# Performance work log

Hardware: AMD Instinct MI355X
Metric: run time of the kernel (lower is better)

Reference implementation:

```python
import jax, jax.numpy as jnp
import numpy as np

B, C, H, W = 16, 256, 96, 96
CQ = C // 8      # 32, query/key channels in CrossAttention
CM = C // 2      # 128, inter_planes


def conv1x1(x, w, b=None):
    # x: [B,Cin,H,W], w: [Cout,Cin]
    y = jnp.einsum('bchw,oc->bohw', x, w)
    if b is not None:
        y = y + b[None, :, None, None]
    return y


def cross_attention(x, wq, bq, wk, bk, wv, bv, gamma):
    # criss-cross (axial H and W) attention with -inf diagonal on the H branch
    b_, c_, h_, w_ = x.shape
    q = conv1x1(x, wq, bq)  # [B,CQ,H,W]
    k = conv1x1(x, wk, bk)
    v = conv1x1(x, wv, bv)  # [B,C,H,W]
    # energy over column (H axis): [B,H,W,H], masked diag h==h'
    e_h = jnp.einsum('bchw,bckw->bhwk', q, k)
    diag = jnp.eye(h_, dtype=bool)[None, :, None, :]  # [1,H,1,H]
    e_h = jnp.where(diag, -jnp.inf, e_h)
    # energy over row (W axis): [B,H,W,W]
    e_w = jnp.einsum('bchw,bchv->bhwv', q, k)
    att = jax.nn.softmax(jnp.concatenate([e_h, e_w], axis=3), axis=3)
    a_h, a_w = att[..., :h_], att[..., h_:]
    out_h = jnp.einsum('bckw,bhwk->bchw', v, a_h)
    out_w = jnp.einsum('bchv,bhwv->bchw', v, a_w)
    return gamma * (out_h + out_w) + x


def spatial_weighted(x, w_q_right, w_v_right, w_up, b_up):
    b_, _, h_, w_ = x.shape
    inp = conv1x1(x, w_v_right).reshape(b_, CM, h_ * w_)        # [B,CM,HW]
    mask = conv1x1(x, w_q_right).reshape(b_, 1, h_ * w_)        # [B,1,HW]
    mask = jax.nn.softmax(mask, axis=2)
    ctx = jnp.einsum('bcn,bon->bco', inp, mask)                 # [B,CM,1]
    ctx = jnp.einsum('bci,oc->boi', ctx, w_up) + b_up[None, :, None]  # [B,C,1]
    mask_ch = jax.nn.sigmoid(ctx)[..., None]                    # [B,C,1,1]
    return x * mask_ch


def channel_weighted(x, w_q_left, w_v_left):
    b_, _, h_, w_ = x.shape
    g = conv1x1(x, w_q_left)                                    # [B,CM,H,W]
    avg = jnp.mean(g, axis=(2, 3))                              # [B,CM]
    theta = conv1x1(x, w_v_left).reshape(b_, CM, h_ * w_)       # [B,CM,HW]
    ctx = jnp.einsum('bc,bcn->bn', avg, theta)                  # [B,HW]
    ctx = jax.nn.softmax(ctx, axis=1).reshape(b_, 1, h_, w_)
    return x * jax.nn.sigmoid(ctx)


def setup_inputs() -> dict:
    key = jax.random.key(0)
    ks = jax.random.split(key, 16)
    s = lambda fan_in: (2.0 / fan_in) ** 0.5
    inp = {
        'x': jax.random.normal(ks[0], (B, C, H, W), jnp.float32),
        'w_q_right': jax.random.normal(ks[1], (1, C), jnp.float32) * s(C),
        'w_v_right': jax.random.normal(ks[2], (CM, C), jnp.float32) * s(C),
        'w_up': jax.random.normal(ks[3], (C, CM), jnp.float32) * s(CM),
        'b_up': jnp.zeros((C,), jnp.float32),
        'w_q_left': jax.random.normal(ks[4], (CM, C), jnp.float32) * s(C),
        'w_v_left': jax.random.normal(ks[5], (CM, C), jnp.float32) * s(C),
        'cr_wq': jax.random.normal(ks[6], (CQ, C), jnp.float32) * s(C),
        'cr_bq': jnp.zeros((CQ,), jnp.float32),
        'cr_wk': jax.random.normal(ks[7], (CQ, C), jnp.float32) * s(C),
        'cr_bk': jnp.zeros((CQ,), jnp.float32),
        'cr_wv': jax.random.normal(ks[8], (C, C), jnp.float32) * s(C),
        'cr_bv': jnp.zeros((C,), jnp.float32),
        'gamma': jax.random.normal(ks[9], (1,), jnp.float32) * 0.1,
    }
    return inp


def reference(x, w_q_right, w_v_right, w_up, b_up, w_q_left, w_v_left,
              cr_wq, cr_bq, cr_wk, cr_bk, cr_wv, cr_bv, gamma):
    cross = lambda t: cross_attention(t, cr_wq, cr_bq, cr_wk, cr_bk, cr_wv, cr_bv, gamma)
    ctx_channel = cross(spatial_weighted(x, w_q_right, w_v_right, w_up, b_up))
    ctx_spatial = cross(channel_weighted(x, w_q_left, w_v_left))
    return cross(ctx_spatial + ctx_channel)
```

## Files before the change

kernel.cpp:

```cpp
#include <hip/hip_runtime.h>
#include <math.h>

#define Bn 16
#define Cn 256
#define Hn 96
#define Wn 96
#define Nn 9216
#define PIXn 147456
#define XSZk ((size_t)Bn*Cn*Nn)
#define YSZk ((size_t)Bn*64*Nn)
#define ATTSZ ((size_t)PIXn*96)

typedef short bf8 __attribute__((ext_vector_type(8)));
typedef float f32x4 __attribute__((ext_vector_type(4)));
#define MFMA(a,b,c) __builtin_amdgcn_mfma_f32_16x16x32_bf16(a,b,c,0,0,0)

typedef unsigned short ushort_t;
typedef _Float16 h16;

__device__ inline ushort_t f2bf(float f){
  union{float f; unsigned int u;} v; v.f=f;
  unsigned int r = v.u + 0x7fffu + ((v.u>>16)&1u);
  return (ushort_t)(r>>16);
}
__device__ inline float bf2f(ushort_t s){
  union{unsigned int u; float f;} v; v.u = ((unsigned int)s)<<16;
  return v.f;
}
__device__ inline ushort_t f2h(float f){
  union{h16 h; ushort_t u;} v; v.h=(h16)f; return v.u;
}
__device__ inline float h2f(ushort_t u){
  union{ushort_t u; h16 h;} v; v.u=u; return (float)v.h;
}

__device__ inline float waveSum(float v){
#pragma unroll
  for(int o=32;o;o>>=1) v += __shfl_down(v,o,64);
  return v;
}
__device__ inline float waveMax(float v){
#pragma unroll
  for(int o=32;o;o>>=1) v = fmaxf(v,__shfl_down(v,o,64));
  return v;
}


template<int XBW>
__global__ __launch_bounds__(1024) void k_pass1(const float* __restrict__ x,
    const float* __restrict__ wqr, float* __restrict__ xmean,
    float* __restrict__ partp, ushort_t* __restrict__ XB){
  int cg = blockIdx.x, b = blockIdx.y, tid = threadIdx.x;
  __shared__ float r16[16];
  float mp[2][8];
#pragma unroll
  for(int u=0;u<2;u++)
#pragma unroll
    for(int e=0;e<8;e++) mp[u][e]=0.f;
  for(int cc=0;cc<16;cc++){
    int c = cg*16+cc;
    const float* row = x + ((size_t)b*Cn + c)*Nn;
    float w = wqr[c];
    float s = 0.f;
#pragma unroll
    for(int u=0;u<2;u++){
      int ch = tid + u*1024;
      if(ch < 1152){
        float4 a = *(const float4*)&row[ch*8];
        float4 d = *(const float4*)&row[ch*8+4];
        float v0=a.x,v1=a.y,v2=a.z,v3=a.w,v4=d.x,v5=d.y,v6=d.z,v7=d.w;
        s += ((v0+v1)+(v2+v3))+((v4+v5)+(v6+v7));
        mp[u][0]+=w*v0; mp[u][1]+=w*v1; mp[u][2]+=w*v2; mp[u][3]+=w*v3;
        mp[u][4]+=w*v4; mp[u][5]+=w*v5; mp[u][6]+=w*v6; mp[u][7]+=w*v7;
        if(XBW){
          uint4 pk;
          pk.x=(unsigned)f2bf(v0)|((unsigned)f2bf(v1)<<16);
          pk.y=(unsigned)f2bf(v2)|((unsigned)f2bf(v3)<<16);
          pk.z=(unsigned)f2bf(v4)|((unsigned)f2bf(v5)<<16);
          pk.w=(unsigned)f2bf(v6)|((unsigned)f2bf(v7)<<16);
          *(uint4*)&XB[((size_t)b*Cn + c)*Nn + ch*8] = pk;
        }
      }
    }
    s = waveSum(s);
    if((tid&63)==0) r16[tid>>6]=s;
    __syncthreads();
    if(tid==0){
      float t=0.f;
      for(int i=0;i<16;i++) t+=r16[i];
      xmean[(size_t)b*Cn + c] = t*(1.f/Nn);
    }
    __syncthreads();
  }
  float* dst = partp + ((size_t)cg*Bn + b)*Nn;
#pragma unroll
  for(int u=0;u<2;u++){
    int ch = tid + u*1024;
    if(ch < 1152){
      float4 o1, o2;
      o1.x=mp[u][0]; o1.y=mp[u][1]; o1.z=mp[u][2]; o1.w=mp[u][3];
      o2.x=mp[u][4]; o2.y=mp[u][5]; o2.z=mp[u][6]; o2.w=mp[u][7];
      *(float4*)&dst[ch*8]   = o1;
      *(float4*)&dst[ch*8+4] = o2;
    }
  }
}

template<int XBR>
__global__ __launch_bounds__(1024) void k_pass2(const float* __restrict__ x,
    const ushort_t* __restrict__ XB, const float* __restrict__ wvec,
    const float* __restrict__ maskb, float* __restrict__ xw,
    float* __restrict__ partp){
  int cg = blockIdx.x, b = blockIdx.y, tid = threadIdx.x;
  __shared__ float r16[16];
  float cp[2][8], mk[2][8];
#pragma unroll
  for(int u=0;u<2;u++){
    int ch = tid + u*1024;
    if(ch < 1152){
      float4 a = *(const float4*)&maskb[(size_t)b*Nn + ch*8];
      float4 d = *(const float4*)&maskb[(size_t)b*Nn + ch*8 + 4];
      mk[u][0]=a.x; mk[u][1]=a.y; mk[u][2]=a.z; mk[u][3]=a.w;
      mk[u][4]=d.x; mk[u][5]=d.y; mk[u][6]=d.z; mk[u][7]=d.w;
    }
#pragma unroll
    for(int e=0;e<8;e++) cp[u][e]=0.f;
  }
  for(int cc=0;cc<16;cc++){
    int c = cg*16+cc;
    float w = wvec[(size_t)b*Cn + c];
    float s = 0.f;
#pragma unroll
    for(int u=0;u<2;u++){
      int ch = tid + u*1024;
      if(ch < 1152){
        float v[8];
        if(XBR){
          uint4 q = *(const uint4*)&XB[((size_t)b*Cn + c)*Nn + ch*8];
          unsigned* qp=(unsigned*)&q;
#pragma unroll
          for(int k=0;k<4;k++){
            v[2*k]   = bf2f((ushort_t)(qp[k]&0xffff));
            v[2*k+1] = bf2f((ushort_t)(qp[k]>>16));
          }
        } else {
          const float* row = x + ((size_t)b*Cn + c)*Nn;
          float4 a = *(const float4*)&row[ch*8];
          float4 d = *(const float4*)&row[ch*8+4];
          v[0]=a.x; v[1]=a.y; v[2]=a.z; v[3]=a.w;
          v[4]=d.x; v[5]=d.y; v[6]=d.z; v[7]=d.w;
        }
#pragma unroll
        for(int e=0;e<8;e++){
          s += mk[u][e]*v[e];
          cp[u][e] += w*v[e];
        }
      }
    }
    s = waveSum(s);
    if((tid&63)==0) r16[tid>>6]=s;
    __syncthreads();
    if(tid==0){
      float t=0.f;
      for(int i=0;i<16;i++) t+=r16[i];
      xw[(size_t)b*Cn + c] = t;
    }
    __syncthreads();
  }
  float* dst = partp + ((size_t)cg*Bn + b)*Nn;
#pragma unroll
  for(int u=0;u<2;u++){
    int ch = tid + u*1024;
    if(ch < 1152){
      float4 o1, o2;
      o1.x=cp[u][0]; o1.y=cp[u][1]; o1.z=cp[u][2]; o1.w=cp[u][3];
      o2.x=cp[u][4]; o2.y=cp[u][5]; o2.z=cp[u][6]; o2.w=cp[u][7];
      *(float4*)&dst[ch*8]   = o1;
      *(float4*)&dst[ch*8+4] = o2;
    }
  }
}

__global__ void k_red16(const float* __restrict__ part, float* __restrict__ out){
  size_t p = (size_t)blockIdx.x*256 + threadIdx.x;
  float s=0.f;
#pragma unroll
  for(int cg=0;cg<16;cg++) s += part[(size_t)cg*Bn*Nn + p];
  out[p]=s;
}

__device__ inline void softmax_n_body(const float* __restrict__ in,
    float* __restrict__ out, int b, int mode){
  int tid=threadIdx.x, lane=tid&63, wid=tid>>6;
  const float* p = in + (size_t)b*Nn;
  __shared__ float red[16];
  __shared__ float bc2[2];
  float mx=-3e38f;
  for(int i=tid;i<Nn;i+=1024) mx=fmaxf(mx,p[i]);
  mx = waveMax(mx);
  if(lane==0) red[wid]=mx;
  __syncthreads();
  if(tid==0){ float m=red[0]; for(int i=1;i<16;i++) m=fmaxf(m,red[i]); bc2[0]=m; }
  __syncthreads();
  mx=bc2[0];
  float s=0.f;
  for(int i=tid;i<Nn;i+=1024) s+=expf(p[i]-mx);
  s = waveSum(s);
  __syncthreads();
  if(lane==0) red[wid]=s;
  __syncthreads();
  if(tid==0){ float t=0.f; for(int i=0;i<16;i++) t+=red[i]; bc2[1]=t; }
  __syncthreads();
  float inv=1.f/bc2[1];
  for(int i=tid;i<Nn;i+=1024){
    float e=expf(p[i]-mx)*inv;
    out[(size_t)b*Nn+i] = mode ? 1.f/(1.f+expf(-e)) : e;
  }
}

__global__ __launch_bounds__(1024) void k_sn1(const float* __restrict__ mraw,
    float* __restrict__ maskb, const float* __restrict__ xmean,
    const float* __restrict__ wql, const float* __restrict__ wvl,
    float* __restrict__ wvec){
  if(blockIdx.x < 16){
    softmax_n_body(mraw, maskb, blockIdx.x, 0);
  } else {
    int b = blockIdx.x - 16, t = threadIdx.x;
    __shared__ float xm[Cn];
    __shared__ float av[128];
    if(t<Cn) xm[t] = xmean[b*Cn+t];
    __syncthreads();
    if(t<128){
      float s=0.f;
      for(int c=0;c<Cn;c++) s += wql[t*Cn+c]*xm[c];
      av[t]=s;
    }
    __syncthreads();
    if(t<Cn){
      float s=0.f;
      for(int m=0;m<128;m++) s += av[m]*wvl[m*Cn+t];
      wvec[b*Cn+t]=s;
    }
  }
}

__global__ __launch_bounds__(1024) void k_sn2(const float* __restrict__ craw,
    float* __restrict__ m2, const float* __restrict__ xw,
    const float* __restrict__ wvr, const float* __restrict__ wup,
    const float* __restrict__ bup, float* __restrict__ g1){
  if(blockIdx.x < 16){
    softmax_n_body(craw, m2, blockIdx.x, 1);
  } else {
    int b = blockIdx.x - 16, t = threadIdx.x;
    __shared__ float xs[Cn];
    __shared__ float cx[128];
    if(t<Cn) xs[t]=xw[b*Cn+t];
    __syncthreads();
    if(t<128){
      float s=0.f;
      for(int c=0;c<Cn;c++) s += wvr[t*Cn+c]*xs[c];
      cx[t]=s;
    }
    __syncthreads();
    if(t<Cn){
      float s=bup[t];
      for(int m=0;m<128;m++) s += wup[t*128+m]*cx[m];
      g1[b*Cn+t]=1.f/(1.f+expf(-s));
    }
  }
}


__global__ void k_packb(const float* __restrict__ wq, const float* __restrict__ bq,
                        const float* __restrict__ wk, const float* __restrict__ bk,
                        const float* __restrict__ wv, const float* __restrict__ bv,
                        ushort_t* __restrict__ Wp, float* __restrict__ bp){
  int o = blockIdx.x, t = threadIdx.x;
  const float* src; float bs;
  if(o<32){ src = wq + o*Cn; bs = bq[o]; }
  else if(o<64){ src = wk + (o-32)*Cn; bs = bk[o-32]; }
  else { src = wv + (o-64)*Cn; bs = bv[o-64]; }
  Wp[o*Cn+t] = f2bf(src[t]);
  if(t==0) bp[o] = bs;
}

#define AP 40
#define BP 264
#define GP 68

template<int GATED, int XBR>
__global__ __launch_bounds__(256) void k_gemm_qkv(
    const ushort_t* __restrict__ tb, const float* __restrict__ x,
    const ushort_t* __restrict__ XBp,
    const float* __restrict__ g1, const float* __restrict__ m2,
    const ushort_t* __restrict__ Wp, const float* __restrict__ bp,
    ushort_t* __restrict__ Yqk, ushort_t* __restrict__ Vb, int sel){
  __shared__ ushort_t SM[320*AP + 64*BP];
  __shared__ float gsh[256];
  ushort_t* Ws = SM;
  ushort_t* Bt = SM + 320*AP;
  int b = blockIdx.y;
  int n0 = blockIdx.x*64;
  int tid = threadIdx.x, lane = tid&63, wid = tid>>6;

  if(GATED){
    gsh[tid] = g1[b*Cn + tid];
    __syncthreads();
    float scl_n = (sel==1) ? m2[(size_t)b*Nn + n0 + (tid&63)] : 0.f;
    int cg = (tid>>6)*8;
#pragma unroll
    for(int p=0;p<8;p++){
      int c8 = p*32 + cg;
      float fv[8];
      if(XBR){
        const ushort_t* xb = XBp + (size_t)b*Cn*Nn + n0 + (tid&63);
#pragma unroll
        for(int k2=0;k2<8;k2++){
          float xf = bf2f(xb[(size_t)(c8+k2)*Nn]);
          fv[k2] = xf * (sel==0 ? gsh[c8+k2] : scl_n);
        }
      } else {
        const float* xb = x + (size_t)b*Cn*Nn + n0 + (tid&63);
#pragma unroll
        for(int k2=0;k2<8;k2++){
          float xf = xb[(size_t)(c8+k2)*Nn];
          fv[k2] = xf * (sel==0 ? gsh[c8+k2] : scl_n);
        }
      }
      uint4 pk;
      pk.x = (unsigned)f2bf(fv[0]) | ((unsigned)f2bf(fv[1])<<16);
      pk.y = (unsigned)f2bf(fv[2]) | ((unsigned)f2bf(fv[3])<<16);
      pk.z = (unsigned)f2bf(fv[4]) | ((unsigned)f2bf(fv[5])<<16);
      pk.w = (unsigned)f2bf(fv[6]) | ((unsigned)f2bf(fv[7])<<16);
      *(uint4*)&Bt[(tid&63)*BP + c8] = pk;
    }
  } else {
    const ushort_t* xb = tb + (size_t)b*Cn*Nn + n0 + (tid&63);
    int cg = (tid>>6)*8;
#pragma unroll
    for(int p=0;p<8;p++){
      int c8 = p*32 + cg;
      unsigned e0=xb[(size_t)(c8+0)*Nn], e1=xb[(size_t)(c8+1)*Nn];
      unsigned e2=xb[(size_t)(c8+2)*Nn], e3=xb[(size_t)(c8+3)*Nn];
      unsigned e4=xb[(size_t)(c8+4)*Nn], e5=xb[(size_t)(c8+5)*Nn];
      unsigned e6=xb[(size_t)(c8+6)*Nn], e7=xb[(size_t)(c8+7)*Nn];
      uint4 pk;
      pk.x = e0 | (e1<<16); pk.y = e2 | (e3<<16);
      pk.z = e4 | (e5<<16); pk.w = e6 | (e7<<16);
      *(uint4*)&Bt[(tid&63)*BP + c8] = pk;
    }
  }

  f32x4 acc[5][4];
#pragma unroll
  for(int f=0;f<5;f++)
#pragma unroll
    for(int g=0;g<4;g++) acc[f][g] = (f32x4){0.f,0.f,0.f,0.f};

  for(int ki=0;ki<8;ki++){
    __syncthreads();
#pragma unroll
    for(int q=0;q<5;q++){
      int fidx = q*256 + tid;
      int o = fidx>>2, kk = (fidx&3)*8;
      uint4 wv = *(const uint4*)&Wp[o*Cn + ki*32 + kk];
      *(uint4*)&Ws[o*AP + kk] = wv;
    }
    __syncthreads();
    bf8 bfr[4];
#pragma unroll
    for(int g=0;g<4;g++)
      bfr[g] = *(const bf8*)&Bt[(g*16 + (lane&15))*BP + ki*32 + (lane>>4)*8];
#pragma unroll
    for(int f=0;f<5;f++){
      bf8 a = *(const bf8*)&Ws[(wid*80 + f*16 + (lane&15))*AP + (lane>>4)*8];
#pragma unroll
      for(int g=0;g<4;g++) acc[f][g] = MFMA(a, bfr[g], acc[f][g]);
    }
  }

  __syncthreads();
#pragma unroll
  for(int f=0;f<5;f++){
    int o = wid*80 + f*16 + (lane>>4)*4;
#pragma unroll
    for(int i=0;i<4;i++){
      float bias = bp[o+i];
#pragma unroll
      for(int g=0;g<4;g++)
        SM[(o+i)*GP + g*16 + (lane&15)] = f2bf(acc[f][g][i] + bias);
    }
  }
  __syncthreads();
  for(int u=tid; u<320*8; u+=256){
    int lo_ = u>>3, c8 = (u&7)*8;
    ushort_t* dst = (lo_<64) ? (Yqk + ((size_t)b*64 + lo_)*Nn)
                             : (Vb + ((size_t)b*Cn + (lo_-64))*Nn);
    *(uint4*)&dst[n0 + c8] = *(uint4*)&SM[lo_*GP + c8];
  }
}

__global__ __launch_bounds__(256) void k_transpose_b(const ushort_t* __restrict__ src,
                                                     ushort_t* __restrict__ dst){
  __shared__ ushort_t Ls[96*98];
  size_t base = (size_t)blockIdx.x * Nn;
  int tid = threadIdx.x;
  for(int e=tid*2; e<Nn; e+=512){
    unsigned int u = *(const unsigned int*)&src[base+e];
    int r=e/96, c=e%96;
    *(unsigned int*)&Ls[r*98+c] = u;
  }
  __syncthreads();
  for(int e=tid*2; e<Nn; e+=512){
    int r=e/96, c=e%96;
    unsigned int u = (unsigned int)Ls[c*98+r] | (((unsigned int)Ls[(c+1)*98+r])<<16);
    *(unsigned int*)&dst[base+e] = u;
  }
}

__global__ __launch_bounds__(256) void k_e2(const ushort_t* __restrict__ Yqk,
    const ushort_t* __restrict__ Yqkt, ushort_t* __restrict__ attl,
    ushort_t* __restrict__ attr){
  __shared__ ushort_t Qt[96*AP];
  __shared__ ushort_t Kt[96*AP];
  int r = blockIdx.x, mode = blockIdx.y, b = blockIdx.z;
  const ushort_t* Y = mode ? Yqk : Yqkt;
  int pm   = mode ? 1  : 96;
  int pr   = mode ? 96 : 1;
  ushort_t* attx = mode ? attr : attl;
  int tid = threadIdx.x, lane = tid&63, wid = tid>>6;
  {
    int half = tid>>7;
    int cg   = (tid>>5)&3;
    int l32  = tid&31;
    ushort_t* T = half ? Kt : Qt;
    const ushort_t* S = Y + ((size_t)b*64 + half*32 + cg*8)*Nn + (size_t)r*96;
#pragma unroll
    for(int p=0;p<3;p++){
      int sp = p*32 + l32;
      unsigned e0=S[(size_t)0*Nn+sp], e1=S[(size_t)1*Nn+sp];
      unsigned e2=S[(size_t)2*Nn+sp], e3=S[(size_t)3*Nn+sp];
      unsigned e4=S[(size_t)4*Nn+sp], e5=S[(size_t)5*Nn+sp];
      unsigned e6=S[(size_t)6*Nn+sp], e7=S[(size_t)7*Nn+sp];
      uint4 pk;
      pk.x = e0 | (e1<<16); pk.y = e2 | (e3<<16);
      pk.z = e4 | (e5<<16); pk.w = e6 | (e7<<16);
      *(uint4*)&T[sp*AP + cg*8] = pk;
    }
  }
  __syncthreads();
  int mb = (wid>>1)*48, nb = (wid&1)*48;
  const f32x4 z4 = {0.f,0.f,0.f,0.f};
  f32x4 acc[3][3];
  bf8 a[3], bb[3];
#pragma unroll
  for(int f=0;f<3;f++) a[f] = *(const bf8*)&Qt[(mb+f*16+(lane&15))*AP + (lane>>4)*8];
#pragma unroll
  for(int g=0;g<3;g++) bb[g] = *(const bf8*)&Kt[(nb+g*16+(lane&15))*AP + (lane>>4)*8];
#pragma unroll
  for(int f=0;f<3;f++)
#pragma unroll
    for(int g=0;g<3;g++) acc[f][g] = MFMA(a[f], bb[g], z4);
#pragma unroll
  for(int f=0;f<3;f++)
#pragma unroll
    for(int i=0;i<4;i++){
      int m = mb + f*16 + (lane>>4)*4 + i;
      ushort_t* arow = attx + ((size_t)b*Nn + (size_t)m*pm + (size_t)r*pr)*96;
#pragma unroll
      for(int g=0;g<3;g++){
        int n = nb + g*16 + (lane&15);
        arow[n] = f2h(acc[f][g][i]);
      }
    }
}

__global__ __launch_bounds__(256) void k_smvt(ushort_t* attl, ushort_t* attr,
    const ushort_t* __restrict__ Vsrc, ushort_t* __restrict__ Vdst){
  __shared__ ushort_t Ls[96*98];
  int b = blockIdx.z;
  if(blockIdx.x < 1164){
    int wave = threadIdx.x>>6, l = threadIdx.x&63;
    int t = blockIdx.x*4 + wave;
    int i=0, base=0;
    while(base + (96-i) <= t){ base += 96-i; i++; }
    int j = i + (t-base);
    int hf = l>>5, l32 = l&31;
    int h = hf ? j : i, w = hf ? i : j;
    size_t p = (size_t)b*Nn + (size_t)h*96 + w;
    const ushort_t* al = attl + p*96;
    const ushort_t* ar = attr + p*96;
    float v[6];
#pragma unroll
    for(int k=0;k<3;k++){
      int el = l32 + 32*k;
      float vv = h2f(al[el]);
      v[k] = (el==h) ? -1e30f : vv;
    }
#pragma unroll
    for(int k=0;k<3;k++) v[3+k] = h2f(ar[l32 + 32*k]);
    float mx = v[0];
#pragma unroll
    for(int k=1;k<6;k++) mx = fmaxf(mx, v[k]);
#pragma unroll
    for(int o=16;o;o>>=1) mx = fmaxf(mx, __shfl_xor(mx, o, 64));
    float e[6], s=0.f;
#pragma unroll
    for(int k=0;k<6;k++){ e[k]=expf(v[k]-mx); s+=e[k]; }
#pragma unroll
    for(int o=16;o;o>>=1) s += __shfl_xor(s, o, 64);
    float inv = 1.f/s;
    size_t q = (size_t)b*Nn + (size_t)w*96 + h;
    ushort_t* oh = attl + q*96;
    ushort_t* ow = attr + p*96;
#pragma unroll
    for(int k=0;k<3;k++) oh[l32+32*k] = f2bf(e[k]*inv);
#pragma unroll
    for(int k=0;k<3;k++) ow[l32+32*k] = f2bf(e[3+k]*inv);
  } else {
    int c = blockIdx.x - 1164;
    size_t base = ((size_t)b*Cn + c) * Nn;
    int tid = threadIdx.x;
    for(int e=tid*2; e<Nn; e+=512){
      unsigned int u = *(const unsigned int*)&Vsrc[base+e];
      int r=e/96, cc=e%96;
      *(unsigned int*)&Ls[r*98+cc] = u;
    }
    __syncthreads();
    for(int e=tid*2; e<Nn; e+=512){
      int r=e/96, cc=e%96;
      unsigned int u = (unsigned int)Ls[cc*98+r] | (((unsigned int)Ls[(cc+1)*98+r])<<16);
      *(unsigned int*)&Vdst[base+e] = u;
    }
  }
}

#define SP 104
#define RP 100

template<int RES, int XBR>
__global__ __launch_bounds__(256) void k_pv2(const ushort_t* __restrict__ VB,
    const ushort_t* __restrict__ VTb, const ushort_t* __restrict__ attw,
    const ushort_t* __restrict__ atth, const float* __restrict__ x,
    const ushort_t* __restrict__ XBp,
    const float* __restrict__ g1, const float* __restrict__ m2,
    const ushort_t* __restrict__ residb, ushort_t* __restrict__ Tob,
    ushort_t* __restrict__ OTb, const float* __restrict__ gp, int sel){
  __shared__ ushort_t SMEM[96*SP];
  int r = blockIdx.x, mode = blockIdx.y>>2, q4 = blockIdx.y&3, b = blockIdx.z;
  float gm = gp[0];
  int tid = threadIdx.x, lane = tid&63, wid = tid>>6;
  const ushort_t* V = mode ? VTb : VB;
  size_t vbase = (size_t)b*Cn*Nn + (size_t)r*96;
  int cb = q4*64 + wid*16;
  const ushort_t* ab = (mode ? atth : attw) + ((size_t)b*Nn + (size_t)r*96)*96;
  for(int u=tid; u<96*12; u+=256){
    int n=u/12, j8=(u%12)*8;
    uint4 qv = *(const uint4*)&ab[n*96 + j8];
    *(uint4*)&SMEM[n*SP + j8] = qv;
  }
  __syncthreads();
  f32x4 acc[6];
#pragma unroll
  for(int g=0;g<6;g++) acc[g] = (f32x4){0.f,0.f,0.f,0.f};
#pragma unroll
  for(int j0=0;j0<3;j0++){
    bf8 vf = *(const bf8*)&V[vbase
        + (size_t)(cb + (lane&15))*Nn + j0*32 + (lane>>4)*8];
    bf8 bfr[6];
#pragma unroll
    for(int g=0;g<6;g++)
      bfr[g] = *(const bf8*)&SMEM[(g*16+(lane&15))*SP + j0*32 + (lane>>4)*8];
#pragma unroll
    for(int g=0;g<6;g++) acc[g] = MFMA(vf, bfr[g], acc[g]);
  }
  __syncthreads();
  {
    int rl = wid*16 + (lane>>4)*4;
#pragma unroll
    for(int i=0;i<4;i++)
#pragma unroll
      for(int g=0;g<6;g++)
        SMEM[(rl+i)*RP + g*16 + (lane&15)] = f2bf(gm*acc[g][i]);
  }
  __syncthreads();
  for(int u=tid; u<64*12; u+=256){
    int rl = u/12, q8 = (u%12)*8;
    int c = q4*64 + rl;
    size_t row = vbase + (size_t)c*Nn;
    uint4 v = *(uint4*)&SMEM[rl*RP + q8];
    if(mode){
      *(uint4*)&OTb[row + q8] = v;
    } else {
      unsigned* vp=(unsigned*)&v;
      float rs[8];
      if(RES==1){
        uint4 rv = *(const uint4*)&residb[row + q8];
        unsigned* rp=(unsigned*)&rv;
#pragma unroll
        for(int k=0;k<4;k++){
          rs[2*k]   = bf2f((ushort_t)(rp[k]&0xffff));
          rs[2*k+1] = bf2f((ushort_t)(rp[k]>>16));
        }
      } else {
        float xv[8];
        if(XBR){
          uint4 xq = *(const uint4*)&XBp[row + q8];
          unsigned* xp=(unsigned*)&xq;
#pragma unroll
          for(int k=0;k<4;k++){
            xv[2*k]   = bf2f((ushort_t)(xp[k]&0xffff));
            xv[2*k+1] = bf2f((ushort_t)(xp[k]>>16));
          }
        } else {
          float4 x1 = *(const float4*)&x[row + q8];
          float4 x2 = *(const float4*)&x[row + q8 + 4];
          xv[0]=x1.x; xv[1]=x1.y; xv[2]=x1.z; xv[3]=x1.w;
          xv[4]=x2.x; xv[5]=x2.y; xv[6]=x2.z; xv[7]=x2.w;
        }
        if(sel==0){
          float g = g1[b*Cn + c];
#pragma unroll
          for(int k=0;k<8;k++) rs[k] = xv[k]*g;
        } else {
          float4 m1 = *(const float4*)&m2[(size_t)b*Nn + (size_t)r*96 + q8];
          float4 m2v= *(const float4*)&m2[(size_t)b*Nn + (size_t)r*96 + q8 + 4];
          float mv[8] = {m1.x,m1.y,m1.z,m1.w,m2v.x,m2v.y,m2v.z,m2v.w};
#pragma unroll
          for(int k=0;k<8;k++) rs[k] = xv[k]*mv[k];
        }
      }
      uint4 o; unsigned* op=(unsigned*)&o;
#pragma unroll
      for(int k=0;k<4;k++){
        float lo = bf2f((ushort_t)(vp[k]&0xffff)) + rs[2*k];
        float hi = bf2f((ushort_t)(vp[k]>>16))    + rs[2*k+1];
        op[k] = (unsigned)f2bf(lo) | ((unsigned)f2bf(hi)<<16);
      }
      *(uint4*)&Tob[row + q8] = o;
    }
  }
}

template<int VAR>
__global__ __launch_bounds__(256) void k_merge(float* __restrict__ outf,
    ushort_t* __restrict__ outb, const ushort_t* __restrict__ add,
    const ushort_t* __restrict__ OT){
  __shared__ ushort_t Ls[96*98];
  size_t base = (size_t)blockIdx.x * Nn;
  int tid = threadIdx.x;
  for(int e=tid*2; e<Nn; e+=512){
    int r=e/96, c=e%96;
    *(unsigned int*)&Ls[r*98+c] = *(const unsigned int*)&OT[base+e];
  }
  __syncthreads();
  for(int e=tid*4; e<Nn; e+=1024){
    int r=e/96, c=e%96;
    float t0 = bf2f(Ls[(c+0)*98+r]), t1 = bf2f(Ls[(c+1)*98+r]);
    float t2 = bf2f(Ls[(c+2)*98+r]), t3 = bf2f(Ls[(c+3)*98+r]);
    if(VAR==4){
      uint2 v = *(const uint2*)&add[base+e];
      float4 o;
      o.x = bf2f((ushort_t)(v.x&0xffff)) + t0;
      o.y = bf2f((ushort_t)(v.x>>16))    + t1;
      o.z = bf2f((ushort_t)(v.y&0xffff)) + t2;
      o.w = bf2f((ushort_t)(v.y>>16))    + t3;
      *(float4*)&outf[base+e] = o;
    } else {
      uint2 u = *(uint2*)&outb[base+e];
      float a0 = bf2f((ushort_t)(u.x&0xffff)) + t0;
      float a1 = bf2f((ushort_t)(u.x>>16))    + t1;
      float a2 = bf2f((ushort_t)(u.y&0xffff)) + t2;
      float a3 = bf2f((ushort_t)(u.y>>16))    + t3;
      if(VAR==2){
        uint2 v = *(const uint2*)&add[base+e];
        a0 += bf2f((ushort_t)(v.x&0xffff));
        a1 += bf2f((ushort_t)(v.x>>16));
        a2 += bf2f((ushort_t)(v.y&0xffff));
        a3 += bf2f((ushort_t)(v.y>>16));
      }
      u.x = (unsigned)f2bf(a0) | ((unsigned)f2bf(a1)<<16);
      u.y = (unsigned)f2bf(a2) | ((unsigned)f2bf(a3)<<16);
      *(uint2*)&outb[base+e] = u;
    }
  }
}

extern "C" void kernel_launch(void* const* d_in, const int* in_sizes, int n_in,
                              void* d_out, int out_size, void* d_ws, size_t ws_size,
                              hipStream_t stream){
  const float* x    = (const float*)d_in[0];
  const float* wqr  = (const float*)d_in[1];
  const float* wvr  = (const float*)d_in[2];
  const float* wup  = (const float*)d_in[3];
  const float* bup  = (const float*)d_in[4];
  const float* wql  = (const float*)d_in[5];
  const float* wvl  = (const float*)d_in[6];
  const float* crwq = (const float*)d_in[7];
  const float* crbq = (const float*)d_in[8];
  const float* crwk = (const float*)d_in[9];
  const float* crbk = (const float*)d_in[10];
  const float* crwv = (const float*)d_in[11];
  const float* crbv = (const float*)d_in[12];
  const float* gma  = (const float*)d_in[13];
  float* out = (float*)d_out;

  char* wsb = (char*)d_ws;
  ushort_t* TT   = (ushort_t*)wsb; wsb += 2*XSZk*2;
  ushort_t* VB2  = (ushort_t*)wsb; wsb += XSZk*2;
  ushort_t* VT2  = (ushort_t*)wsb; wsb += XSZk*2;
  ushort_t* Y2   = (ushort_t*)wsb; wsb += YSZk*2;
  ushort_t* Yt2  = (ushort_t*)wsb; wsb += YSZk*2;
  ushort_t* ATTL = (ushort_t*)wsb; wsb += ATTSZ*2;
  ushort_t* ATTR = (ushort_t*)wsb; wsb += ATTSZ*2;
  float*    partp= (float*)wsb;    wsb += (size_t)16*Bn*Nn*4;
  ushort_t* Wpb  = (ushort_t*)wsb; wsb += 320*Cn*2;
  float*    bp   = (float*)wsb;    wsb += 320*4;
  float*    xmean= (float*)wsb;    wsb += Bn*Cn*4;
  float*    wvec = (float*)wsb;    wsb += Bn*Cn*4;
  float*    xw   = (float*)wsb;    wsb += Bn*Cn*4;
  float*    g1   = (float*)wsb;    wsb += Bn*Cn*4;
  float*    mraw = (float*)wsb;    wsb += (size_t)PIXn*4;
  float*    maskb= (float*)wsb;    wsb += (size_t)PIXn*4;
  float*    craw = (float*)wsb;    wsb += (size_t)PIXn*4;
  float*    m2   = (float*)wsb;    wsb += (size_t)PIXn*4;
  ushort_t* XB   = (ushort_t*)wsb;
  const int useXB = (ws_size >= (size_t)484000000) ? 1 : 0;

  k_packb<<<320,256,0,stream>>>(crwq,crbq,crwk,crbk,crwv,crbv,Wpb,bp);

  if(useXB) k_pass1<1><<<dim3(16,Bn),1024,0,stream>>>(x, wqr, xmean, partp, XB);
  else      k_pass1<0><<<dim3(16,Bn),1024,0,stream>>>(x, wqr, xmean, partp, nullptr);
  k_red16<<<Bn*Nn/256,256,0,stream>>>(partp, mraw);
  k_sn1<<<32,1024,0,stream>>>(mraw, maskb, xmean, wql, wvl, wvec);
  if(useXB) k_pass2<1><<<dim3(16,Bn),1024,0,stream>>>(nullptr, XB, wvec, maskb, xw, partp);
  else      k_pass2<0><<<dim3(16,Bn),1024,0,stream>>>(x, nullptr, wvec, maskb, xw, partp);
  k_red16<<<Bn*Nn/256,256,0,stream>>>(partp, craw);
  k_sn2<<<32,1024,0,stream>>>(craw, m2, xw, wvr, wup, bup, g1);

  ushort_t* T2p = TT + XSZk;

  auto crossg = [&](int sel){
    if(useXB) k_gemm_qkv<1,1><<<dim3(Nn/64,Bn),256,0,stream>>>(nullptr, nullptr, XB, g1, m2, Wpb, bp, Y2, VB2, sel);
    else      k_gemm_qkv<1,0><<<dim3(Nn/64,Bn),256,0,stream>>>(nullptr, x, nullptr, g1, m2, Wpb, bp, Y2, VB2, sel);
    k_transpose_b<<<Bn*64,256,0,stream>>>(Y2, Yt2);
    k_e2<<<dim3(96,2,Bn),256,0,stream>>>(Y2, Yt2, ATTL, ATTR);
    k_smvt<<<dim3(1164+256,1,Bn),256,0,stream>>>(ATTL, ATTR, VB2, VT2);
    ushort_t* To = TT + (size_t)sel*XSZk;
    if(useXB) k_pv2<0,1><<<dim3(96,8,Bn),256,0,stream>>>(VB2, VT2, ATTR, ATTL, nullptr, XB, g1, m2, nullptr, To, VT2, gma, sel);
    else      k_pv2<0,0><<<dim3(96,8,Bn),256,0,stream>>>(VB2, VT2, ATTR, ATTL, x, nullptr, g1, m2, nullptr, To, VT2, gma, sel);
  };

  crossg(0);
  k_merge<0><<<Bn*Cn,256,0,stream>>>(nullptr, TT, nullptr, VT2);
  crossg(1);
  k_merge<2><<<Bn*Cn,256,0,stream>>>(nullptr, TT, T2p, VT2);

  k_gemm_qkv<0,0><<<dim3(Nn/64,Bn),256,0,stream>>>(TT, nullptr, nullptr, nullptr, nullptr, Wpb, bp, Y2, VB2, 0);
  k_transpose_b<<<Bn*64,256,0,stream>>>(Y2, Yt2);
  k_e2<<<dim3(96,2,Bn),256,0,stream>>>(Y2, Yt2, ATTL, ATTR);
  k_smvt<<<dim3(1164+256,1,Bn),256,0,stream>>>(ATTL, ATTR, VB2, VT2);
  k_pv2<1,0><<<dim3(96,8,Bn),256,0,stream>>>(VB2, VT2, ATTR, ATTL,
      nullptr, nullptr, nullptr, nullptr, TT, T2p, VT2, gma, 0);
  k_merge<4><<<Bn*Cn,256,0,stream>>>(out, nullptr, T2p, VT2);
}
```

Baseline: 1.051 ms.

## Read QKV weights directly from global and chunk epilogue to shrink LDS

The QKV projection GEMM no longer stages weight tiles through shared memory each k-step. Each wave now loads its A fragments straight from global/L2, which removes two barriers per iteration. The output epilogue is split into three passes that reuse the small B-tile buffer, so shared memory drops from about 59KB to about 34KB and more blocks can fit per CU. The cost is uncoalesced-ish direct global loads of weights per wave, some extra barriers in the epilogue, and more index arithmetic.

New measurement: 1.104 ms. 1.05x slower.

```diff
diff --git a/kernel.cpp b/kernel.cpp
--- a/kernel.cpp
+++ b/kernel.cpp
@@ -295,10 +295,9 @@
     const float* __restrict__ g1, const float* __restrict__ m2,
     const ushort_t* __restrict__ Wp, const float* __restrict__ bp,
     ushort_t* __restrict__ Yqk, ushort_t* __restrict__ Vb, int sel){
-  __shared__ ushort_t SM[320*AP + 64*BP];
+  __shared__ ushort_t SM[64*BP];
   __shared__ float gsh[256];
-  ushort_t* Ws = SM;
-  ushort_t* Bt = SM + 320*AP;
+  ushort_t* Bt = SM;
   int b = blockIdx.y;
   int n0 = blockIdx.x*64;
   int tid = threadIdx.x, lane = tid&63, wid = tid>>6;
@@ -357,46 +356,49 @@
 #pragma unroll
     for(int g=0;g<4;g++) acc[f][g] = (f32x4){0.f,0.f,0.f,0.f};
 
+  __syncthreads();
   for(int ki=0;ki<8;ki++){
-    __syncthreads();
-#pragma unroll
-    for(int q=0;q<5;q++){
-      int fidx = q*256 + tid;
-      int o = fidx>>2, kk = (fidx&3)*8;
-      uint4 wv = *(const uint4*)&Wp[o*Cn + ki*32 + kk];
-      *(uint4*)&Ws[o*AP + kk] = wv;
-    }
-    __syncthreads();
     bf8 bfr[4];
 #pragma unroll
     for(int g=0;g<4;g++)
       bfr[g] = *(const bf8*)&Bt[(g*16 + (lane&15))*BP + ki*32 + (lane>>4)*8];
 #pragma unroll
     for(int f=0;f<5;f++){
-      bf8 a = *(const bf8*)&Ws[(wid*80 + f*16 + (lane&15))*AP + (lane>>4)*8];
+      bf8 a = *(const bf8*)&Wp[(size_t)(wid*80 + f*16 + (lane&15))*Cn
+                               + ki*32 + (lane>>4)*8];
 #pragma unroll
       for(int g=0;g<4;g++) acc[f][g] = MFMA(a, bfr[g], acc[f][g]);
     }
   }
 
-  __syncthreads();
-#pragma unroll
-  for(int f=0;f<5;f++){
-    int o = wid*80 + f*16 + (lane>>4)*4;
-#pragma unroll
-    for(int i=0;i<4;i++){
-      float bias = bp[o+i];
-#pragma unroll
-      for(int g=0;g<4;g++)
-        SM[(o+i)*GP + g*16 + (lane&15)] = f2bf(acc[f][g][i] + bias);
-    }
-  }
-  __syncthreads();
-  for(int u=tid; u<320*8; u+=256){
-    int lo_ = u>>3, c8 = (u&7)*8;
-    ushort_t* dst = (lo_<64) ? (Yqk + ((size_t)b*64 + lo_)*Nn)
-                             : (Vb + ((size_t)b*Cn + (lo_-64))*Nn);
-    *(uint4*)&dst[n0 + c8] = *(uint4*)&SM[lo_*GP + c8];
+#pragma unroll
+  for(int p=0;p<3;p++){
+    const int nf = (p==2) ? 1 : 2;
+    __syncthreads();
+#pragma unroll
+    for(int ff=0; ff<2; ff++){
+      if(ff < nf){
+        int f = p*2 + ff;
+        int rl = wid*(nf*16) + ff*16 + (lane>>4)*4;
+        int ob = wid*80 + f*16 + (lane>>4)*4;
+#pragma unroll
+        for(int i=0;i<4;i++){
+          float bias = bp[ob+i];
+#pragma unroll
+          for(int g=0;g<4;g++)
+            SM[(rl+i)*GP + g*16 + (lane&15)] = f2bf(acc[f][g][i] + bias);
+        }
+      }
+    }
+    __syncthreads();
+    int nrows = nf*64;
+    for(int u=tid; u<nrows*8; u+=256){
+      int lo_ = u>>3, c8 = (u&7)*8;
+      int o = (lo_/(nf*16))*80 + p*32 + (lo_%(nf*16));
+      ushort_t* dst = (o<64) ? (Yqk + ((size_t)b*64 + o)*Nn)
+                             : (Vb + ((size_t)b*Cn + (o-64))*Nn);
+      *(uint4*)&dst[n0 + c8] = *(uint4*)&SM[lo_*GP + c8];
+    }
   }
 }
 
```
